# Optimization experiments

Measured on AMD Instinct MI355X. Metric: run time of the kernel, lower is better.

The kernel has to match this reference:

```python
import jax, jax.numpy as jnp
import numpy as np

B, S, D, H, E, K, F = 1, 1024, 1024, 16, 8, 2, 4096


def setup_inputs() -> dict:
    key = jax.random.key(0)
    ks = jax.random.split(key, 8)
    n = lambda k, shape, sc: (jax.random.normal(k, shape, dtype=jnp.float32) * sc)
    return {
        "x": n(ks[0], (B, S, D), 1.0),
        "w_qkv": n(ks[1], (D, 3 * D), D ** -0.5),
        "w_o": n(ks[2], (D, D), D ** -0.5),
        "g1": jnp.ones((D,), jnp.float32),
        "b1": jnp.zeros((D,), jnp.float32),
        "wg": n(ks[3], (D, E), D ** -0.5),
        "w1": n(ks[4], (E, D, F), D ** -0.5),
        "bb1": jnp.zeros((E, F), jnp.float32),
        "w2": n(ks[5], (E, F, D), F ** -0.5),
        "bb2": jnp.zeros((E, D), jnp.float32),
        "g2": jnp.ones((D,), jnp.float32),
        "b2": jnp.zeros((D,), jnp.float32),
    }


def layernorm(x, g, b, eps=1e-5):
    m = x.mean(-1, keepdims=True)
    v = ((x - m) ** 2).mean(-1, keepdims=True)
    return (x - m) * jax.lax.rsqrt(v + eps) * g + b


def reference(x, w_qkv, w_o, g1, b1, wg, w1, bb1, w2, bb2, g2, b2):
    b, s, d = x.shape
    hd = d // H
    # --- multi-head causal self-attention ---
    qkv = x @ w_qkv  # [b,s,3d]
    q, k, v = jnp.split(qkv, 3, axis=-1)
    to_heads = lambda t: t.reshape(b, s, H, hd).transpose(0, 2, 1, 3)  # [b,h,s,hd]
    q, k, v = to_heads(q), to_heads(k), to_heads(v)
    scores = jnp.einsum("bhqd,bhkd->bhqk", q, k) / jnp.sqrt(jnp.float32(hd))
    causal = jnp.tril(jnp.ones((s, s), bool))
    scores = jnp.where(causal, scores, jnp.finfo(scores.dtype).min)
    attn = jax.nn.softmax(scores, axis=-1)
    o = jnp.einsum("bhqk,bhkd->bhqd", attn, v)
    o = o.transpose(0, 2, 1, 3).reshape(b, s, d) @ w_o
    # --- add & norm ---
    h = layernorm(x + o, g1, b1)
    # --- MoE FFN: softmax router, top-k, renormalized combine ---
    probs = jax.nn.softmax(h @ wg, axis=-1)  # [b,s,E]
    topv, topi = jax.lax.top_k(probs, K)
    topv = topv / topv.sum(-1, keepdims=True)
    w = (topv[..., None] * jax.nn.one_hot(topi, E, dtype=h.dtype)).sum(-2)  # [b,s,E]
    h1 = jax.nn.gelu(jnp.einsum("bsd,edf->ebsf", h, w1) + bb1[:, None, None, :])
    y = jnp.einsum("ebsf,efd->ebsd", h1, w2) + bb2[:, None, None, :]
    moe = jnp.einsum("ebsd,bse->bsd", y, w)
    # --- residual + norm of MoE block ---
    return layernorm(h + moe, g2, b2)
```

## Files before the change

kernel.cpp:

```cpp
#include <hip/hip_runtime.h>
#include <hip/hip_bf16.h>
#include <math.h>

#define SEQ 1024
#define DIM 1024
#define NH  16
#define NE  8
#define FF  4096

typedef float f32x4 __attribute__((ext_vector_type(4)));
typedef short short8 __attribute__((ext_vector_type(8)));
typedef short s16x4 __attribute__((ext_vector_type(4)));

#define WAIT_VM(N) asm volatile("s_waitcnt vmcnt(" #N ")" ::: "memory")

__device__ __forceinline__ ushort f2bf(float f) {
  union { float f; unsigned u; } v; v.f = f;
  unsigned r = v.u + 0x7FFF + ((v.u >> 16) & 1);
  return (ushort)(r >> 16);
}
__device__ __forceinline__ float bf2f(ushort h) {
  union { unsigned u; float f; } v; v.u = ((unsigned)h) << 16;
  return v.f;
}

__device__ __forceinline__ float gelu_tanh(float x) {
  return 0.5f * x * (1.f + tanhf(0.7978845608028654f * (x + 0.044715f * x * x * x)));
}
__device__ __forceinline__ float gelu_fast(float x) {
  float u = 1.5957691216057308f * (x + 0.044715f * x * x * x);
  return x / (1.f + __expf(-u));
}

__device__ __forceinline__ void gl2lds16(const void* g, void* l) {
  __builtin_amdgcn_global_load_lds(
      (const __attribute__((address_space(1))) unsigned int*)g,
      (__attribute__((address_space(3))) unsigned int*)l, 16, 0, 0);
}

__global__ __launch_bounds__(256) void wconv_kernel(
    const float* __restrict__ wq, const float* __restrict__ wo,
    ushort* __restrict__ wqT, ushort* __restrict__ wqTl,
    ushort* __restrict__ woT, ushort* __restrict__ woTl) {
  __shared__ __align__(16) ushort th[64 * 64];
  __shared__ __align__(16) ushort tl[64 * 64];
  int z = blockIdx.z, t = threadIdx.x;
  const float* src; ushort* dh; ushort* dl; int R, C, r0, c0;
  if (z == 0) {
    src = wq; dh = wqT; dl = wqTl;
    R = DIM; C = 3 * DIM; r0 = blockIdx.y * 64; c0 = blockIdx.x * 64;
  } else {
    if (blockIdx.x >= 16) return;
    src = wo; dh = woT; dl = woTl;
    R = DIM; C = DIM; r0 = blockIdx.y * 64; c0 = blockIdx.x * 64;
  }
  int ry = (t >> 4) * 4;
  int cx = (t & 15) * 4;
  f32x4 v[4];
#pragma unroll
  for (int j = 0; j < 4; j++)
    v[j] = *(const f32x4*)&src[(size_t)(r0 + ry + j) * C + c0 + cx];
#pragma unroll
  for (int i = 0; i < 4; i++) {
    int trow = cx + i;
    int o = trow * 64 + (((ry >> 3) ^ (trow & 7)) << 3) + (ry & 7);
    ushort uh[4], ul[4];
#pragma unroll
    for (int j = 0; j < 4; j++) {
      float f = v[j][i];
      ushort hh = f2bf(f);
      uh[j] = hh;
      ul[j] = f2bf(f - bf2f(hh));
    }
    *(s16x4*)&th[o] = *(const s16x4*)uh;
    *(s16x4*)&tl[o] = *(const s16x4*)ul;
  }
  __syncthreads();
  int tr = t >> 2, tc = (t & 3) * 16;
  int b0 = (tc >> 3) ^ (tr & 7);
  int b1 = ((tc >> 3) + 1) ^ (tr & 7);
  size_t dbase = (size_t)(c0 + tr) * R + r0 + tc;
  short8 u0 = *(const short8*)&th[tr * 64 + b0 * 8];
  short8 u1 = *(const short8*)&th[tr * 64 + b1 * 8];
  *(short8*)&dh[dbase] = u0;
  *(short8*)&dh[dbase + 8] = u1;
  short8 l0 = *(const short8*)&tl[tr * 64 + b0 * 8];
  short8 l1 = *(const short8*)&tl[tr * 64 + b1 * 8];
  *(short8*)&dl[dbase] = l0;
  *(short8*)&dl[dbase + 8] = l1;
}

__global__ __launch_bounds__(256) void bfsplit_kernel(const float* __restrict__ in,
                                                      ushort* __restrict__ oh,
                                                      ushort* __restrict__ ol) {
  int i = (blockIdx.x * 256 + threadIdx.x) * 4;
  f32x4 v = *(const f32x4*)&in[i];
  ushort h[4], l[4];
#pragma unroll
  for (int j = 0; j < 4; j++) { h[j] = f2bf(v[j]); l[j] = f2bf(v[j] - bf2f(h[j])); }
  *(s16x4*)&oh[i] = *(const s16x4*)h;
  *(s16x4*)&ol[i] = *(const s16x4*)l;
}

#define MM_FEXP_LOAD(ra0v, ra1v, rb0v, rb1v, rb2v, rb3v, T)            \
  { int _ko = (T) * 32;                                                \
    ra0v = *(const short8*)(aG[0] + _ko);                              \
    ra1v = *(const short8*)(aG[1] + _ko);                              \
    rb0v = *(const f32x4*)(bG + (size_t)(_ko + 0) * N);                \
    rb1v = *(const f32x4*)(bG + (size_t)(_ko + 1) * N);                \
    rb2v = *(const f32x4*)(bG + (size_t)(_ko + 2) * N);                \
    rb3v = *(const f32x4*)(bG + (size_t)(_ko + 3) * N); }

#define MM_FEXP_STAGE(buf, ra0v, ra1v, rb0v, rb1v, rb2v, rb3v)         \
  { *(short8*)&As[buf][aw[0]] = ra0v;                                  \
    *(short8*)&As[buf][aw[1]] = ra1v;                                  \
    _Pragma("unroll")                                                  \
    for (int i = 0; i < 4; i++) {                                      \
      ushort u[4];                                                     \
      u[0] = f2bf(rb0v[i]); u[1] = f2bf(rb1v[i]);                      \
      u[2] = f2bf(rb2v[i]); u[3] = f2bf(rb3v[i]);                      \
      *(s16x4*)&Bs[buf][(nb * 4 + i) * 40 + bslot * 4] = *(const s16x4*)u; } }

#define MM_FEXP_MFMA(buf)                                              \
  { short8 af[4], bf[4];                                               \
    _Pragma("unroll")                                                  \
    for (int mi = 0; mi < 4; mi++) af[mi] = *(const short8*)&As[buf][aro[mi]]; \
    _Pragma("unroll")                                                  \
    for (int ni = 0; ni < 4; ni++) bf[ni] = *(const short8*)&Bs[buf][bro[ni]]; \
    _Pragma("unroll")                                                  \
    for (int mi = 0; mi < 4; mi++)                                     \
      _Pragma("unroll")                                                \
      for (int ni = 0; ni < 4; ni++)                                   \
        acc[mi][ni] = __builtin_amdgcn_mfma_f32_16x16x32_bf16(af[mi], bf[ni], acc[mi][ni], 0, 0, 0); }

template <int EPI, int KSPLIT>
__global__ __launch_bounds__(256) void mm_fexp(
    const ushort* __restrict__ A, const float* __restrict__ Bf,
    const float* __restrict__ bias, void* __restrict__ Cout,
    const int* __restrict__ tok, const int* __restrict__ offcnt,
    int N, int K)
{
  int zz = blockIdx.z;
  int e  = (KSPLIT > 1) ? (zz & (NE - 1)) : zz;
  int ks = (KSPLIT > 1) ? (zz >> 3) : 0;
  int off = offcnt[e], cnt = offcnt[NE + e];
  int m0 = blockIdx.y * 128;
  if (m0 >= cnt) return;
  int n0 = blockIdx.x * 128;
  const float* Bp = Bf + (size_t)e * K * N;
  const int Kc = K / KSPLIT, kbase = ks * Kc;

  __shared__ __align__(16) ushort As[2][128 * 32];
  __shared__ __align__(16) ushort Bs[2][128 * 40];

  int t = threadIdx.x, lane = t & 63, w = t >> 6, wr = w >> 1, wc = w & 1;

  const ushort* aG[2]; int aw[2];
#pragma unroll
  for (int c = 0; c < 2; c++) {
    int gid = w * 128 + c * 64 + lane;
    int m = gid >> 2, p = gid & 3;
    int kg = p ^ ((m >> 1) & 3);
    int mc = m0 + m; if (mc > cnt - 1) mc = cnt - 1;
    int arow = tok ? tok[off + mc] : (off + mc);
    aG[c] = A + (size_t)arow * K + kbase + kg * 8;
    aw[c] = gid * 8;
  }

  int kb = t >> 5, nb = t & 31;
  const float* bG = Bp + (size_t)(kbase + kb * 4) * N + n0 + nb * 4;
  int bslot = kb ^ ((nb & 3) << 1);

  int aro[4], bro[4];
#pragma unroll
  for (int mi = 0; mi < 4; mi++) {
    int m = wr * 64 + mi * 16 + (lane & 15);
    aro[mi] = (m * 4 + ((lane >> 4) ^ ((m >> 1) & 3))) * 8;
  }
#pragma unroll
  for (int ni = 0; ni < 4; ni++) {
    int n = wc * 64 + ni * 16 + (lane & 15);
    bro[ni] = n * 40 + ((((lane >> 4) * 2) ^ (((n >> 2) & 3) << 1))) * 4;
  }

  f32x4 acc[4][4] = {};
  const int nt = Kc / 32;

  short8 raA0, raA1, raB0, raB1;
  f32x4 rbA0, rbA1, rbA2, rbA3, rbB0, rbB1, rbB2, rbB3;
  MM_FEXP_LOAD(raA0, raA1, rbA0, rbA1, rbA2, rbA3, 0);
  MM_FEXP_LOAD(raB0, raB1, rbB0, rbB1, rbB2, rbB3, 1);

  for (int tt = 0; tt < nt; tt += 2) {
    MM_FEXP_STAGE(0, raA0, raA1, rbA0, rbA1, rbA2, rbA3);
    if (tt + 2 < nt) MM_FEXP_LOAD(raA0, raA1, rbA0, rbA1, rbA2, rbA3, tt + 2);
    asm volatile("s_waitcnt lgkmcnt(0)" ::: "memory");
    __builtin_amdgcn_sched_barrier(0);
    __builtin_amdgcn_s_barrier();
    MM_FEXP_MFMA(0);
    MM_FEXP_STAGE(1, raB0, raB1, rbB0, rbB1, rbB2, rbB3);
    if (tt + 3 < nt) MM_FEXP_LOAD(raB0, raB1, rbB0, rbB1, rbB2, rbB3, tt + 3);
    asm volatile("s_waitcnt lgkmcnt(0)" ::: "memory");
    __builtin_amdgcn_sched_barrier(0);
    __builtin_amdgcn_s_barrier();
    MM_FEXP_MFMA(1);
  }

  const float* biasp = (EPI == 3) ? nullptr : bias + (size_t)e * N;
  float* Cp = (float*)Cout + (size_t)ks * 2048 * N;
#pragma unroll
  for (int mi = 0; mi < 4; mi++) {
#pragma unroll
    for (int j = 0; j < 4; j++) {
      int grow = m0 + wr * 64 + mi * 16 + (lane >> 4) * 4 + j;
      if (grow >= cnt) continue;
      size_t rbase = (size_t)(off + grow) * N;
#pragma unroll
      for (int ni = 0; ni < 4; ni++) {
        int gcol = n0 + wc * 64 + ni * 16 + (lane & 15);
        float v = acc[mi][ni][j];
        if (EPI == 1) ((ushort*)Cout)[rbase + gcol] = f2bf(gelu_fast(v + biasp[gcol]));
        else          Cp[rbase + gcol] = v;
      }
    }
  }
}

#undef MM_FEXP_LOAD
#undef MM_FEXP_STAGE
#undef MM_FEXP_MFMA

__global__ __launch_bounds__(256) void mm_split(
    const ushort* __restrict__ Ah, const ushort* __restrict__ Al,
    const ushort* __restrict__ Bh, const ushort* __restrict__ Bl,
    float* __restrict__ C, int N, int K)
{
  int m0 = blockIdx.y * 128;
  int n0 = blockIdx.x * 128;

  __shared__ __align__(16) ushort Ahs[2][4096], Als[2][4096];
  __shared__ __align__(16) ushort Bhs[2][4096], Bls[2][4096];

  int t = threadIdx.x, lane = t & 63, w = t >> 6, wr = w >> 1, wc = w & 1;

  const ushort *aGh[2], *aGl[2], *bGh[2], *bGl[2];
  int lofs[2];
#pragma unroll
  for (int c = 0; c < 2; c++) {
    int gid = w * 128 + c * 64 + lane;
    int m = gid >> 2, p = gid & 3;
    int kg = p ^ ((m >> 1) & 3);
    aGh[c] = Ah + (size_t)(m0 + m) * K + kg * 8;
    aGl[c] = Al + (size_t)(m0 + m) * K + kg * 8;
    bGh[c] = Bh + (size_t)(n0 + m) * K + kg * 8;
    bGl[c] = Bl + (size_t)(n0 + m) * K + kg * 8;
    lofs[c] = (w * 128 + c * 64) * 8;
  }

  int aro[4], bro[4];
#pragma unroll
  for (int mi = 0; mi < 4; mi++) {
    int m = wr * 64 + mi * 16 + (lane & 15);
    aro[mi] = (m * 4 + ((lane >> 4) ^ ((m >> 1) & 3))) * 8;
  }
#pragma unroll
  for (int ni = 0; ni < 4; ni++) {
    int n = wc * 64 + ni * 16 + (lane & 15);
    bro[ni] = (n * 4 + ((lane >> 4) ^ ((n >> 1) & 3))) * 8;
  }

  f32x4 acc[4][4] = {};
  const int nt = K / 32;

#pragma unroll
  for (int c = 0; c < 2; c++) {
    gl2lds16(aGh[c], &Ahs[0][lofs[c]]); gl2lds16(aGl[c], &Als[0][lofs[c]]);
    gl2lds16(bGh[c], &Bhs[0][lofs[c]]); gl2lds16(bGl[c], &Bls[0][lofs[c]]);
  }
  if (nt > 1) {
#pragma unroll
    for (int c = 0; c < 2; c++) {
      gl2lds16(aGh[c] + 32, &Ahs[1][lofs[c]]); gl2lds16(aGl[c] + 32, &Als[1][lofs[c]]);
      gl2lds16(bGh[c] + 32, &Bhs[1][lofs[c]]); gl2lds16(bGl[c] + 32, &Bls[1][lofs[c]]);
    }
  }

  for (int tt = 0; tt < nt; tt++) {
    if (tt + 1 < nt) WAIT_VM(8); else WAIT_VM(0);
    __builtin_amdgcn_s_barrier();
    int b = tt & 1;
    short8 ah[4], al_[4], bh[4], bl_[4];
#pragma unroll
    for (int mi = 0; mi < 4; mi++) {
      ah[mi] = *(const short8*)&Ahs[b][aro[mi]];
      al_[mi] = *(const short8*)&Als[b][aro[mi]];
    }
#pragma unroll
    for (int ni = 0; ni < 4; ni++) {
      bh[ni] = *(const short8*)&Bhs[b][bro[ni]];
      bl_[ni] = *(const short8*)&Bls[b][bro[ni]];
    }
#pragma unroll
    for (int mi = 0; mi < 4; mi++)
#pragma unroll
      for (int ni = 0; ni < 4; ni++) {
        acc[mi][ni] = __builtin_amdgcn_mfma_f32_16x16x32_bf16(al_[mi], bh[ni], acc[mi][ni], 0, 0, 0);
        acc[mi][ni] = __builtin_amdgcn_mfma_f32_16x16x32_bf16(ah[mi], bl_[ni], acc[mi][ni], 0, 0, 0);
        acc[mi][ni] = __builtin_amdgcn_mfma_f32_16x16x32_bf16(ah[mi], bh[ni], acc[mi][ni], 0, 0, 0);
      }
    asm volatile("s_waitcnt lgkmcnt(0)" ::: "memory");
    __builtin_amdgcn_sched_barrier(0);
    __builtin_amdgcn_s_barrier();
    if (tt + 2 < nt) {
      int ko = (tt + 2) * 32;
#pragma unroll
      for (int c = 0; c < 2; c++) {
        gl2lds16(aGh[c] + ko, &Ahs[b][lofs[c]]); gl2lds16(aGl[c] + ko, &Als[b][lofs[c]]);
        gl2lds16(bGh[c] + ko, &Bhs[b][lofs[c]]); gl2lds16(bGl[c] + ko, &Bls[b][lofs[c]]);
      }
    }
  }

#pragma unroll
  for (int mi = 0; mi < 4; mi++)
#pragma unroll
    for (int j = 0; j < 4; j++) {
      int grow = m0 + wr * 64 + mi * 16 + (lane >> 4) * 4 + j;
      size_t rbase = (size_t)grow * N;
#pragma unroll
      for (int ni = 0; ni < 4; ni++) {
        int gcol = n0 + wc * 64 + ni * 16 + (lane & 15);
        C[rbase + gcol] = acc[mi][ni][j];
      }
    }
}

template <int EPI, int SPLIT>
__global__ __launch_bounds__(256) void mm_bf16(
    const float* __restrict__ A, const float* __restrict__ B,
    const float* __restrict__ bias, float* __restrict__ C,
    const int* __restrict__ tok, const int* __restrict__ offcnt,
    int M, int N, int K)
{
  int e = blockIdx.z;
  int off = 0, cnt = M;
  if (offcnt) { off = offcnt[e]; cnt = offcnt[NE + e]; }
  int m0 = blockIdx.y * 128;
  if (m0 >= cnt) return;
  const float* Bp = B + (size_t)e * K * N;
  const float* biasp = (EPI == 0) ? nullptr : bias + (size_t)e * N;
  int n0 = blockIdx.x * 128;

  __shared__ __align__(16) ushort As[(SPLIT + 1) * 128 * 32];
  __shared__ __align__(16) ushort Bs[(SPLIT + 1) * 128 * 32];

  int t = threadIdx.x;
  int lane = t & 63;
  int w = t >> 6, wr = w >> 1, wc = w & 1;

  const float* aptr[2];
  int aws[2];
  for (int i = 0; i < 2; i++) {
    int mr = i * 64 + (t >> 2);
    int mc = m0 + mr; if (mc > cnt - 1) mc = cnt - 1;
    int arow = tok ? tok[off + mc] : (off + mc);
    aptr[i] = A + (size_t)arow * K + (t & 3) * 8;
    aws[i] = mr * 32 + (t & 3) * 8;
  }

  int bn = t >> 1, bkh = (t & 1) * 16;
  const float* bptr = Bp + (size_t)bkh * N + n0 + bn;
  int bws0 = bn * 32 + 8 * (((bkh >> 3) + 0) ^ (bn & 3));
  int bws1 = bn * 32 + 8 * (((bkh >> 3) + 1) ^ (bn & 3));

  int aro[4], bro[4];
#pragma unroll
  for (int mi = 0; mi < 4; mi++)
    aro[mi] = (wr * 64 + mi * 16 + (lane & 15)) * 32 + (lane >> 4) * 8;
#pragma unroll
  for (int ni = 0; ni < 4; ni++) {
    int n = wc * 64 + ni * 16 + (lane & 15);
    bro[ni] = n * 32 + 8 * ((lane >> 4) ^ (n & 3));
  }

  f32x4 acc[4][4] = {};

  for (int k0 = 0; k0 < K; k0 += 32) {
#pragma unroll
    for (int i = 0; i < 2; i++) {
      f32x4 v0 = *(const f32x4*)(aptr[i] + k0);
      f32x4 v1 = *(const f32x4*)(aptr[i] + k0 + 4);
      ushort uh[8], ul[8];
#pragma unroll
      for (int j = 0; j < 4; j++) {
        float f0 = v0[j], f1 = v1[j];
        ushort h0 = f2bf(f0), h1 = f2bf(f1);
        uh[j] = h0; uh[4 + j] = h1;
        if (SPLIT) { ul[j] = f2bf(f0 - bf2f(h0)); ul[4 + j] = f2bf(f1 - bf2f(h1)); }
      }
      *(short8*)&As[aws[i]] = *(const short8*)uh;
      if (SPLIT) *(short8*)&As[4096 + aws[i]] = *(const short8*)ul;
    }
    {
      const float* bp = bptr + (size_t)k0 * N;
      ushort uh[16], ul[16];
#pragma unroll
      for (int i = 0; i < 16; i++) {
        float f = bp[(size_t)i * N];
        ushort h = f2bf(f);
        uh[i] = h;
        if (SPLIT) ul[i] = f2bf(f - bf2f(h));
      }
      *(short8*)&Bs[bws0] = *(const short8*)&uh[0];
      *(short8*)&Bs[bws1] = *(const short8*)&uh[8];
      if (SPLIT) {
        *(short8*)&Bs[4096 + bws0] = *(const short8*)&ul[0];
        *(short8*)&Bs[4096 + bws1] = *(const short8*)&ul[8];
      }
    }
    __syncthreads();
    short8 afh[4], bfh[4], afl[4], bfl[4];
#pragma unroll
    for (int mi = 0; mi < 4; mi++) {
      afh[mi] = *(const short8*)&As[aro[mi]];
      if (SPLIT) afl[mi] = *(const short8*)&As[4096 + aro[mi]];
    }
#pragma unroll
    for (int ni = 0; ni < 4; ni++) {
      bfh[ni] = *(const short8*)&Bs[bro[ni]];
      if (SPLIT) bfl[ni] = *(const short8*)&Bs[4096 + bro[ni]];
    }
#pragma unroll
    for (int mi = 0; mi < 4; mi++)
#pragma unroll
      for (int ni = 0; ni < 4; ni++) {
        if (SPLIT) {
          acc[mi][ni] = __builtin_amdgcn_mfma_f32_16x16x32_bf16(afl[mi], bfh[ni], acc[mi][ni], 0, 0, 0);
          acc[mi][ni] = __builtin_amdgcn_mfma_f32_16x16x32_bf16(afh[mi], bfl[ni], acc[mi][ni], 0, 0, 0);
        }
        acc[mi][ni] = __builtin_amdgcn_mfma_f32_16x16x32_bf16(afh[mi], bfh[ni], acc[mi][ni], 0, 0, 0);
      }
    __syncthreads();
  }

#pragma unroll
  for (int mi = 0; mi < 4; mi++) {
#pragma unroll
    for (int j = 0; j < 4; j++) {
      int grow = m0 + wr * 64 + mi * 16 + (lane >> 4) * 4 + j;
      if (grow >= cnt) continue;
      size_t rbase = (size_t)(off + grow) * N;
#pragma unroll
      for (int ni = 0; ni < 4; ni++) {
        int gcol = n0 + wc * 64 + ni * 16 + (lane & 15);
        float v = acc[mi][ni][j];
        if (EPI >= 1) v += biasp[gcol];
        if (EPI == 1) v = gelu_tanh(v);
        C[rbase + gcol] = v;
      }
    }
  }
}

__device__ __forceinline__ int vidx(int d, int key) {
  return d * 64 + ((((key >> 3) ^ (d & 7)) << 3) | (key & 7));
}

__global__ __launch_bounds__(256, 1) void attn_mfma(const float* __restrict__ qkv,
                                                    float* __restrict__ o) {
  const int qb = blockIdx.x;
  const int head = blockIdx.y;
  const int q0 = qb * 128;
  const int t = threadIdx.x;
  const int lane = t & 63, w = t >> 6;
  const int g = lane >> 4, l4 = lane & 15;

  __shared__ __align__(16) ushort Kh[64 * 64], Kl[64 * 64];
  __shared__ __align__(16) ushort Vh[64 * 64], Vl[64 * 64];
  __shared__ __align__(16) ushort Ph[4][32 * 72], Pl[4][32 * 72];

  short8 qh[2][2], ql[2][2];
#pragma unroll
  for (int mi = 0; mi < 2; mi++)
#pragma unroll
    for (int ks = 0; ks < 2; ks++) {
      int row = q0 + w * 32 + mi * 16 + l4;
      const float* qp = qkv + (size_t)row * 3072 + head * 64 + ks * 32 + g * 8;
      f32x4 a = *(const f32x4*)qp;
      f32x4 b4 = *(const f32x4*)(qp + 4);
      ushort uh[8], ul_[8];
#pragma unroll
      for (int j = 0; j < 4; j++) {
        ushort h0 = f2bf(a[j]), h1 = f2bf(b4[j]);
        uh[j] = h0; uh[4 + j] = h1;
        ul_[j] = f2bf(a[j] - bf2f(h0)); ul_[4 + j] = f2bf(b4[j] - bf2f(h1));
      }
      qh[mi][ks] = *(const short8*)uh;
      ql[mi][ks] = *(const short8*)ul_;
    }

  float m_s[2][4], l_s[2][4];
  f32x4 O[2][4] = {};
#pragma unroll
  for (int mi = 0; mi < 2; mi++)
#pragma unroll
    for (int j = 0; j < 4; j++) { m_s[mi][j] = -INFINITY; l_s[mi][j] = 0.f; }

  const int nt = 2 * (qb + 1);
  for (int kt = 0; kt < nt; kt++) {
    const int kv0 = kt * 64;
    __syncthreads();
    {
      int key = t >> 2;
      int dblk = (t & 3) * 16;
      const float* kp = qkv + (size_t)(kv0 + key) * 3072 + 1024 + head * 64 + dblk;
      const float* vp = kp + 1024;
      f32x4 k0 = *(const f32x4*)kp, k1 = *(const f32x4*)(kp + 4),
            k2 = *(const f32x4*)(kp + 8), k3 = *(const f32x4*)(kp + 12);
      f32x4 v0 = *(const f32x4*)vp, v1 = *(const f32x4*)(vp + 4),
            v2 = *(const f32x4*)(vp + 8), v3 = *(const f32x4*)(vp + 12);
      float kf[16] = {k0[0],k0[1],k0[2],k0[3], k1[0],k1[1],k1[2],k1[3],
                      k2[0],k2[1],k2[2],k2[3], k3[0],k3[1],k3[2],k3[3]};
      float vf[16] = {v0[0],v0[1],v0[2],v0[3], v1[0],v1[1],v1[2],v1[3],
                      v2[0],v2[1],v2[2],v2[3], v3[0],v3[1],v3[2],v3[3]};
#pragma unroll
      for (int half = 0; half < 2; half++) {
        int d8 = (dblk >> 3) + half;
        int idx = key * 64 + ((d8 ^ (key & 7)) << 3);
        ushort uh[8], ul_[8];
#pragma unroll
        for (int j = 0; j < 8; j++) {
          float f = kf[half * 8 + j];
          ushort h = f2bf(f);
          uh[j] = h; ul_[j] = f2bf(f - bf2f(h));
        }
        *(short8*)&Kh[idx] = *(const short8*)uh;
        *(short8*)&Kl[idx] = *(const short8*)ul_;
      }
#pragma unroll
      for (int i = 0; i < 16; i++) {
        int d = dblk + i;
        int idx = vidx(d, key);
        float f = vf[i];
        ushort h = f2bf(f);
        Vh[idx] = h; Vl[idx] = f2bf(f - bf2f(h));
      }
    }
    __syncthreads();

    if (kv0 <= q0 + w * 32 + 31) {
      f32x4 S[2][4] = {};
#pragma unroll
      for (int ks = 0; ks < 2; ks++) {
        short8 kbh[4], kbl[4];
#pragma unroll
        for (int ni = 0; ni < 4; ni++) {
          int key = ni * 16 + l4;
          int d8 = ks * 4 + g;
          int idx = key * 64 + ((d8 ^ (key & 7)) << 3);
          kbh[ni] = *(const short8*)&Kh[idx];
          kbl[ni] = *(const short8*)&Kl[idx];
        }
#pragma unroll
        for (int mi = 0; mi < 2; mi++)
#pragma unroll
          for (int ni = 0; ni < 4; ni++) {
            S[mi][ni] = __builtin_amdgcn_mfma_f32_16x16x32_bf16(ql[mi][ks], kbh[ni], S[mi][ni], 0, 0, 0);
            S[mi][ni] = __builtin_amdgcn_mfma_f32_16x16x32_bf16(qh[mi][ks], kbl[ni], S[mi][ni], 0, 0, 0);
            S[mi][ni] = __builtin_amdgcn_mfma_f32_16x16x32_bf16(qh[mi][ks], kbh[ni], S[mi][ni], 0, 0, 0);
          }
      }
#pragma unroll
      for (int mi = 0; mi < 2; mi++) {
        int rowb = q0 + w * 32 + mi * 16 + g * 4;
        float mx[4] = {-INFINITY, -INFINITY, -INFINITY, -INFINITY};
#pragma unroll
        for (int ni = 0; ni < 4; ni++) {
          int col = kv0 + ni * 16 + l4;
#pragma unroll
          for (int j = 0; j < 4; j++) {
            float s = S[mi][ni][j] * 0.125f;
            if (col > rowb + j) s = -INFINITY;
            S[mi][ni][j] = s;
            mx[j] = fmaxf(mx[j], s);
          }
        }
#pragma unroll
        for (int j = 0; j < 4; j++) {
#pragma unroll
          for (int msk = 8; msk; msk >>= 1) mx[j] = fmaxf(mx[j], __shfl_xor(mx[j], msk));
          float mn = fmaxf(m_s[mi][j], mx[j]);
          float sc = __expf(m_s[mi][j] - mn);
          m_s[mi][j] = mn;
          l_s[mi][j] *= sc;
#pragma unroll
          for (int df = 0; df < 4; df++) O[mi][df][j] *= sc;
        }
        float ps[4] = {0.f, 0.f, 0.f, 0.f};
#pragma unroll
        for (int ni = 0; ni < 4; ni++)
#pragma unroll
          for (int j = 0; j < 4; j++) {
            float p = __expf(S[mi][ni][j] - m_s[mi][j]);
            ps[j] += p;
            int rl = mi * 16 + g * 4 + j, cl = ni * 16 + l4;
            ushort h = f2bf(p);
            Ph[w][rl * 72 + cl] = h;
            Pl[w][rl * 72 + cl] = f2bf(p - bf2f(h));
          }
#pragma unroll
        for (int j = 0; j < 4; j++) {
#pragma unroll
          for (int msk = 8; msk; msk >>= 1) ps[j] += __shfl_xor(ps[j], msk);
          l_s[mi][j] += ps[j];
        }
      }
      asm volatile("s_waitcnt lgkmcnt(0)" ::: "memory");
      __builtin_amdgcn_sched_barrier(0);
#pragma unroll
      for (int ks = 0; ks < 2; ks++) {
        short8 pah[2], pal[2], vbh[4], vbl[4];
#pragma unroll
        for (int mi = 0; mi < 2; mi++) {
          int idx = (mi * 16 + l4) * 72 + ks * 32 + g * 8;
          pah[mi] = *(const short8*)&Ph[w][idx];
          pal[mi] = *(const short8*)&Pl[w][idx];
        }
#pragma unroll
        for (int df = 0; df < 4; df++) {
          int d = df * 16 + l4;
          int k8 = ks * 4 + g;
          int idx = d * 64 + ((k8 ^ (d & 7)) << 3);
          vbh[df] = *(const short8*)&Vh[idx];
          vbl[df] = *(const short8*)&Vl[idx];
        }
#pragma unroll
        for (int mi = 0; mi < 2; mi++)
#pragma unroll
          for (int df = 0; df < 4; df++) {
            O[mi][df] = __builtin_amdgcn_mfma_f32_16x16x32_bf16(pal[mi], vbh[df], O[mi][df], 0, 0, 0);
            O[mi][df] = __builtin_amdgcn_mfma_f32_16x16x32_bf16(pah[mi], vbl[df], O[mi][df], 0, 0, 0);
            O[mi][df] = __builtin_amdgcn_mfma_f32_16x16x32_bf16(pah[mi], vbh[df], O[mi][df], 0, 0, 0);
          }
      }
    }
  }

#pragma unroll
  for (int mi = 0; mi < 2; mi++)
#pragma unroll
    for (int j = 0; j < 4; j++) {
      int row = q0 + w * 32 + mi * 16 + g * 4 + j;
      float inv = 1.f / l_s[mi][j];
#pragma unroll
      for (int df = 0; df < 4; df++)
        o[(size_t)row * DIM + head * 64 + df * 16 + l4] = O[mi][df][j] * inv;
    }
}

__device__ float block_reduce_256(float v, float* red, int t) {
  red[t] = v; __syncthreads();
  for (int st = 128; st > 0; st >>= 1) {
    if (t < st) red[t] += red[t + st];
    __syncthreads();
  }
  float r = red[0];
  __syncthreads();
  return r;
}

__global__ __launch_bounds__(256) void addln_kernel(const float* __restrict__ x,
                                                    const float* __restrict__ r,
                                                    const float* __restrict__ g,
                                                    const float* __restrict__ b,
                                                    float* __restrict__ out,
                                                    ushort* __restrict__ outb) {
  __shared__ float red[256];
  int row = blockIdx.x, t = threadIdx.x;
  float vals[4];
  float s = 0.f;
  for (int i = 0; i < 4; i++) {
    int d = t + i * 256;
    vals[i] = x[(size_t)row * DIM + d] + r[(size_t)row * DIM + d];
    s += vals[i];
  }
  float mean = block_reduce_256(s, red, t) * (1.f / DIM);
  float vs = 0.f;
  for (int i = 0; i < 4; i++) { float d = vals[i] - mean; vs += d * d; }
  float var = block_reduce_256(vs, red, t) * (1.f / DIM);
  float inv = rsqrtf(var + 1e-5f);
  for (int i = 0; i < 4; i++) {
    int d = t + i * 256;
    float v = (vals[i] - mean) * inv * g[d] + b[d];
    out[(size_t)row * DIM + d] = v;
    if (outb) outb[(size_t)row * DIM + d] = f2bf(v);
  }
}

__global__ __launch_bounds__(256) void router_kernel(const float* __restrict__ h,
                                                     const float* __restrict__ wg,
                                                     int* __restrict__ topi,
                                                     float* __restrict__ topw) {
  __shared__ float red[NE][256];
  int tkn = blockIdx.x, t = threadIdx.x;
  float acc[NE] = {};
  for (int i = 0; i < 4; i++) {
    int d = t + i * 256;
    float hv = h[(size_t)tkn * DIM + d];
    const float* wr = wg + (size_t)d * NE;
    for (int e = 0; e < NE; e++) acc[e] += hv * wr[e];
  }
  for (int e = 0; e < NE; e++) red[e][t] = acc[e];
  __syncthreads();
  for (int st = 128; st > 0; st >>= 1) {
    if (t < st)
      for (int e = 0; e < NE; e++) red[e][t] += red[e][t + st];
    __syncthreads();
  }
  if (t == 0) {
    float l[NE];
    for (int e = 0; e < NE; e++) l[e] = red[e][0];
    int i0 = 0;
    for (int e = 1; e < NE; e++) if (l[e] > l[i0]) i0 = e;
    int i1 = -1;
    for (int e = 0; e < NE; e++) {
      if (e == i0) continue;
      if (i1 < 0 || l[e] > l[i1]) i1 = e;
    }
    float p1 = __expf(l[i1] - l[i0]);
    float inv = 1.f / (1.f + p1);
    topi[tkn * 2] = i0; topi[tkn * 2 + 1] = i1;
    topw[tkn * 2] = inv; topw[tkn * 2 + 1] = p1 * inv;
  }
}

__global__ __launch_bounds__(1024) void compact_kernel(const int* __restrict__ topi,
                                                       int* __restrict__ tok,
                                                       int* __restrict__ assign_row,
                                                       int* __restrict__ offcnt) {
  __shared__ int scan[1024];
  __shared__ int sbase;
  int t = threadIdx.x;
  if (t == 0) sbase = 0;
  __syncthreads();
  for (int e = 0; e < NE; e++) {
    int which = -1;
    if (topi[t * 2] == e) which = 0;
    else if (topi[t * 2 + 1] == e) which = 1;
    scan[t] = (which >= 0) ? 1 : 0;
    __syncthreads();
    for (int s2 = 1; s2 < 1024; s2 <<= 1) {
      int add = (t >= s2) ? scan[t - s2] : 0;
      __syncthreads();
      scan[t] += add;
      __syncthreads();
    }
    int incl = scan[t];
    int total = scan[1023];
    int base = sbase;
    if (which >= 0) {
      int pos = base + incl - 1;
      tok[pos] = t;
      assign_row[t * 2 + which] = pos;
    }
    if (t == 0) { offcnt[e] = base; offcnt[NE + e] = total; }
    __syncthreads();
    if (t == 0) sbase = base + total;
    __syncthreads();
  }
}

template <int KS>
__global__ __launch_bounds__(256) void final_ln_kernel(const float* __restrict__ h,
                                                       const float* __restrict__ y,
                                                       const int* __restrict__ assign_row,
                                                       const float* __restrict__ topw,
                                                       const int* __restrict__ topi,
                                                       const float* __restrict__ bb2,
                                                       const float* __restrict__ g,
                                                       const float* __restrict__ b,
                                                       float* __restrict__ out) {
  __shared__ float red[256];
  int row = blockIdx.x, t = threadIdx.x;
  int r0 = assign_row[row * 2], r1 = assign_row[row * 2 + 1];
  float w0 = topw[row * 2], w1 = topw[row * 2 + 1];
  float vals[4];
  float s = 0.f;
  for (int i = 0; i < 4; i++) {
    int d = t + i * 256;
    float acc0 = 0.f, acc1 = 0.f;
#pragma unroll
    for (int p = 0; p < KS; p++) {
      acc0 += y[(size_t)p * 2048 * DIM + (size_t)r0 * DIM + d];
      acc1 += y[(size_t)p * 2048 * DIM + (size_t)r1 * DIM + d];
    }
    float v = h[(size_t)row * DIM + d] + w0 * acc0 + w1 * acc1;
    if (KS > 1) {
      int e0 = topi[row * 2], e1 = topi[row * 2 + 1];
      v += w0 * bb2[e0 * DIM + d] + w1 * bb2[e1 * DIM + d];
    }
    vals[i] = v;
    s += v;
  }
  float mean = block_reduce_256(s, red, t) * (1.f / DIM);
  float vs = 0.f;
  for (int i = 0; i < 4; i++) { float d = vals[i] - mean; vs += d * d; }
  float var = block_reduce_256(vs, red, t) * (1.f / DIM);
  float inv = rsqrtf(var + 1e-5f);
  for (int i = 0; i < 4; i++) {
    int d = t + i * 256;
    out[(size_t)row * DIM + d] = (vals[i] - mean) * inv * g[d] + b[d];
  }
}

extern "C" void kernel_launch(void* const* d_in, const int* in_sizes, int n_in,
                              void* d_out, int out_size, void* d_ws, size_t ws_size,
                              hipStream_t stream) {
  const float* x     = (const float*)d_in[0];
  const float* w_qkv = (const float*)d_in[1];
  const float* w_o   = (const float*)d_in[2];
  const float* g1    = (const float*)d_in[3];
  const float* b1    = (const float*)d_in[4];
  const float* wg    = (const float*)d_in[5];
  const float* w1    = (const float*)d_in[6];
  const float* bb1   = (const float*)d_in[7];
  const float* w2    = (const float*)d_in[8];
  const float* bb2   = (const float*)d_in[9];
  const float* g2    = (const float*)d_in[10];
  const float* b2    = (const float*)d_in[11];
  float* out = (float*)d_out;
  float* ws = (float*)d_ws;

  const bool fast = ws_size >= (size_t)46671872 * 4;

  if (fast) {
    float* qkv    = ws;
    float* attn_o = ws + 3145728;
    float* oproj  = ws + 4194304;
    float* h      = ws + 5242880;
    float* ybuf   = ws + 6291456;
    float* topw   = ws + 8388608;
    int*   ibase  = (int*)(ws + 8390656);
    int* topi       = ibase;
    int* tok        = ibase + 2048;
    int* assign_row = ibase + 4096;
    int* offcnt     = ibase + 6144;
    ushort* hb  = (ushort*)(ws + 8398848);
    ushort* h1b = (ushort*)(ws + 8923136);
    ushort* wqT  = (ushort*)(ws + 13117440);
    ushort* wqTl = wqT + 3145728;
    ushort* woT  = wqT + 6291456;
    ushort* woTl = wqT + 7340032;
    float* ypart = ws + 17311744;
    ushort* xh = (ushort*)ybuf;
    ushort* xl = xh + 1048576;
    ushort* oh = xh + 2097152;
    ushort* ol = xh + 3145728;

    wconv_kernel<<<dim3(48, 16, 2), 256, 0, stream>>>(w_qkv, w_o,
                                                      wqT, wqTl, woT, woTl);
    bfsplit_kernel<<<dim3(SEQ * DIM / 1024), 256, 0, stream>>>(x, xh, xl);
    mm_split<<<dim3(24, 8), 256, 0, stream>>>(xh, xl, wqT, wqTl, qkv, 3 * DIM, DIM);
    attn_mfma<<<dim3(8, NH), 256, 0, stream>>>(qkv, attn_o);
    bfsplit_kernel<<<dim3(SEQ * DIM / 1024), 256, 0, stream>>>(attn_o, oh, ol);
    mm_split<<<dim3(8, 8), 256, 0, stream>>>(oh, ol, woT, woTl, oproj, DIM, DIM);
    addln_kernel<<<dim3(SEQ), 256, 0, stream>>>(x, oproj, g1, b1, h, hb);
    router_kernel<<<dim3(SEQ), 256, 0, stream>>>(h, wg, topi, topw);
    compact_kernel<<<dim3(1), 1024, 0, stream>>>(topi, tok, assign_row, offcnt);
    mm_fexp<1, 1><<<dim3(FF / 128, 8, NE), 256, 0, stream>>>(hb, w1, bb1, (void*)h1b,
                                                             tok, offcnt, FF, DIM);
    mm_fexp<3, 4><<<dim3(DIM / 128, 8, NE * 4), 256, 0, stream>>>(h1b, w2, nullptr,
                                                                  (void*)ypart,
                                                                  nullptr, offcnt, DIM, FF);
    final_ln_kernel<4><<<dim3(SEQ), 256, 0, stream>>>(h, ypart, assign_row, topw,
                                                      topi, bb2, g2, b2, out);
  } else {
    float* qkv    = ws;
    float* attn_o = ws + 3145728;
    float* oproj  = ws + 4194304;
    float* h      = ws + 5242880;
    float* h1     = ws + 6291456;
    float* ybuf   = ws + 14680064;
    float* topw   = ws + 16777216;
    int*   ibase  = (int*)(ws + 16779264);
    int* topi       = ibase;
    int* tok        = ibase + 2048;
    int* assign_row = ibase + 4096;
    int* offcnt     = ibase + 6144;

    mm_bf16<0, 1><<<dim3(24, 8, 1), 256, 0, stream>>>(x, w_qkv, nullptr, qkv,
                                                      nullptr, nullptr, SEQ, 3 * DIM, DIM);
    attn_mfma<<<dim3(8, NH), 256, 0, stream>>>(qkv, attn_o);
    mm_bf16<0, 1><<<dim3(8, 8, 1), 256, 0, stream>>>(attn_o, w_o, nullptr, oproj,
                                                     nullptr, nullptr, SEQ, DIM, DIM);
    addln_kernel<<<dim3(SEQ), 256, 0, stream>>>(x, oproj, g1, b1, h, nullptr);
    router_kernel<<<dim3(SEQ), 256, 0, stream>>>(h, wg, topi, topw);
    compact_kernel<<<dim3(1), 1024, 0, stream>>>(topi, tok, assign_row, offcnt);
    mm_bf16<1, 0><<<dim3(32, 8, NE), 256, 0, stream>>>(h, w1, bb1, h1,
                                                       tok, offcnt, SEQ, FF, DIM);
    mm_bf16<2, 0><<<dim3(8, 8, NE), 256, 0, stream>>>(h1, w2, bb2, ybuf,
                                                      nullptr, offcnt, SEQ, DIM, FF);
    final_ln_kernel<1><<<dim3(SEQ), 256, 0, stream>>>(h, ybuf, assign_row, topw,
                                                      nullptr, nullptr, g2, b2, out);
  }
}
```

Measured before the change: 338.7 us.

## Split attention KV range into two chunks with a separate combine kernel

The attention kernel now splits each query block's causal KV range into two halves, launched as separate blocks (grid 8x2x16 instead of 8x16). Each block writes unnormalized partial outputs plus running max and sum. A new combine kernel merges them with log-sum-exp rescaling. This doubles the block count and halves the longest per-block loop, improving load balance and occupancy on a GPU with many CUs, at the cost of an extra kernel launch and extra global traffic for the partials. -INFINITY is replaced by -1e30 so empty or masked chunks do not produce NaNs.

Result: faster. 313.5 us (-7.4%).

```diff
diff --git a/kernel.cpp b/kernel.cpp
--- a/kernel.cpp
+++ b/kernel.cpp
@@ -9,6 +9,7 @@
 #define FF  4096
 
 typedef float f32x4 __attribute__((ext_vector_type(4)));
+typedef float f32x2 __attribute__((ext_vector_type(2)));
 typedef short short8 __attribute__((ext_vector_type(8)));
 typedef short s16x4 __attribute__((ext_vector_type(4)));
 
@@ -467,9 +468,11 @@
 }
 
 __global__ __launch_bounds__(256, 1) void attn_mfma(const float* __restrict__ qkv,
-                                                    float* __restrict__ o) {
+                                                    float* __restrict__ opart,
+                                                    float* __restrict__ ml) {
   const int qb = blockIdx.x;
-  const int head = blockIdx.y;
+  const int ch = blockIdx.y;
+  const int head = blockIdx.z;
   const int q0 = qb * 128;
   const int t = threadIdx.x;
   const int lane = t & 63, w = t >> 6;
@@ -504,10 +507,11 @@
 #pragma unroll
   for (int mi = 0; mi < 2; mi++)
 #pragma unroll
-    for (int j = 0; j < 4; j++) { m_s[mi][j] = -INFINITY; l_s[mi][j] = 0.f; }
-
-  const int nt = 2 * (qb + 1);
-  for (int kt = 0; kt < nt; kt++) {
+    for (int j = 0; j < 4; j++) { m_s[mi][j] = -1e30f; l_s[mi][j] = 0.f; }
+
+  const int kt_beg = ch ? (qb + 1) : 0;
+  const int kt_end = ch ? 2 * (qb + 1) : (qb + 1);
+  for (int kt = kt_beg; kt < kt_end; kt++) {
     const int kv0 = kt * 64;
     __syncthreads();
     {
@@ -573,14 +577,14 @@
 #pragma unroll
       for (int mi = 0; mi < 2; mi++) {
         int rowb = q0 + w * 32 + mi * 16 + g * 4;
-        float mx[4] = {-INFINITY, -INFINITY, -INFINITY, -INFINITY};
+        float mx[4] = {-1e30f, -1e30f, -1e30f, -1e30f};
 #pragma unroll
         for (int ni = 0; ni < 4; ni++) {
           int col = kv0 + ni * 16 + l4;
 #pragma unroll
           for (int j = 0; j < 4; j++) {
             float s = S[mi][ni][j] * 0.125f;
-            if (col > rowb + j) s = -INFINITY;
+            if (col > rowb + j) s = -1e30f;
             S[mi][ni][j] = s;
             mx[j] = fmaxf(mx[j], s);
           }
@@ -651,11 +655,36 @@
 #pragma unroll
     for (int j = 0; j < 4; j++) {
       int row = q0 + w * 32 + mi * 16 + g * 4 + j;
-      float inv = 1.f / l_s[mi][j];
+      if (l4 == 0) {
+        float* mlp = ml + (((size_t)ch * NH + head) * SEQ + row) * 2;
+        mlp[0] = m_s[mi][j];
+        mlp[1] = l_s[mi][j];
+      }
 #pragma unroll
       for (int df = 0; df < 4; df++)
-        o[(size_t)row * DIM + head * 64 + df * 16 + l4] = O[mi][df][j] * inv;
-    }
+        opart[(size_t)ch * (SEQ * DIM) + (size_t)row * DIM + head * 64 + df * 16 + l4] =
+            O[mi][df][j];
+    }
+}
+
+__global__ __launch_bounds__(256) void attn_combine(const float* __restrict__ opart,
+                                                    const float* __restrict__ ml,
+                                                    float* __restrict__ o) {
+  int row = blockIdx.x, t = threadIdx.x;
+  int d0 = t * 4;
+  int head = d0 >> 6;
+  const float* p0 = ml + (((size_t)0 * NH + head) * SEQ + row) * 2;
+  const float* p1 = ml + (((size_t)1 * NH + head) * SEQ + row) * 2;
+  float m0 = p0[0], l0 = p0[1], m1 = p1[0], l1 = p1[1];
+  float M = fmaxf(m0, m1);
+  float w0 = __expf(m0 - M), w1 = __expf(m1 - M);
+  float inv = 1.f / (l0 * w0 + l1 * w1);
+  f32x4 O0 = *(const f32x4*)&opart[(size_t)row * DIM + d0];
+  f32x4 O1 = *(const f32x4*)&opart[(size_t)(SEQ * DIM) + (size_t)row * DIM + d0];
+  f32x4 r;
+#pragma unroll
+  for (int j = 0; j < 4; j++) r[j] = (O0[j] * w0 + O1[j] * w1) * inv;
+  *(f32x4*)&o[(size_t)row * DIM + d0] = r;
 }
 
 __device__ float block_reduce_256(float v, float* red, int t) {
@@ -856,12 +885,15 @@
     ushort* xl = xh + 1048576;
     ushort* oh = xh + 2097152;
     ushort* ol = xh + 3145728;
+    float* opart = ypart;
+    float* mlbuf = ypart + 2097152;
 
     wconv_kernel<<<dim3(48, 16, 2), 256, 0, stream>>>(w_qkv, w_o,
                                                       wqT, wqTl, woT, woTl);
     bfsplit_kernel<<<dim3(SEQ * DIM / 1024), 256, 0, stream>>>(x, xh, xl);
     mm_split<<<dim3(24, 8), 256, 0, stream>>>(xh, xl, wqT, wqTl, qkv, 3 * DIM, DIM);
-    attn_mfma<<<dim3(8, NH), 256, 0, stream>>>(qkv, attn_o);
+    attn_mfma<<<dim3(8, 2, NH), 256, 0, stream>>>(qkv, opart, mlbuf);
+    attn_combine<<<dim3(SEQ), 256, 0, stream>>>(opart, mlbuf, attn_o);
     bfsplit_kernel<<<dim3(SEQ * DIM / 1024), 256, 0, stream>>>(attn_o, oh, ol);
     mm_split<<<dim3(8, 8), 256, 0, stream>>>(oh, ol, woT, woTl, oproj, DIM, DIM);
     addln_kernel<<<dim3(SEQ), 256, 0, stream>>>(x, oproj, g1, b1, h, hb);
@@ -887,10 +919,13 @@
     int* tok        = ibase + 2048;
     int* assign_row = ibase + 4096;
     int* offcnt     = ibase + 6144;
+    float* opart = h1;
+    float* mlbuf = h1 + 2097152;
 
     mm_bf16<0, 1><<<dim3(24, 8, 1), 256, 0, stream>>>(x, w_qkv, nullptr, qkv,
                                                       nullptr, nullptr, SEQ, 3 * DIM, DIM);
-    attn_mfma<<<dim3(8, NH), 256, 0, stream>>>(qkv, attn_o);
+    attn_mfma<<<dim3(8, 2, NH), 256, 0, stream>>>(qkv, opart, mlbuf);
+    attn_combine<<<dim3(SEQ), 256, 0, stream>>>(opart, mlbuf, attn_o);
     mm_bf16<0, 1><<<dim3(8, 8, 1), 256, 0, stream>>>(attn_o, w_o, nullptr, oproj,
                                                      nullptr, nullptr, SEQ, DIM, DIM);
     addln_kernel<<<dim3(SEQ), 256, 0, stream>>>(x, oproj, g1, b1, h, nullptr);
```
